# Kernel optimization log

Hardware: AMD Instinct MI355X
Metric: run time of the kernel (lower is better)

The kernel has to match this reference:

```python
import jax, jax.numpy as jnp
import numpy as np

B, C, H, W = 4, 128, 64, 64
HEADS, DH, MEM = 4, 32, 16
HID = HEADS * DH  # 128


def setup_inputs() -> dict:
    key = jax.random.key(0)
    k1, k2, k3, k4, k5 = jax.random.split(key, 5)
    return {
        "x": jax.random.normal(k1, (B, C, H, W), jnp.float32),
        "memory": jax.random.normal(k2, (1, C, 1, MEM), jnp.float32),
        "w_qkv": jax.random.normal(k3, (3 * HID, C), jnp.float32) * 0.05,  # conv1x1, bias=False
        "w_out": jax.random.normal(k4, (C, HID), jnp.float32) * 0.05,      # conv1x1 weight
        "b_out": jax.random.normal(k5, (C,), jnp.float32) * 0.01,          # conv1x1 bias
    }


def reference(x, memory, w_qkv, w_out, b_out):
    b, c, h, w = x.shape
    hw = h * w
    scale = DH ** -0.5

    # flatten spatial, append memory tokens along token axis
    x_flat = x.reshape(b, c, hw)                         # (b, c, hw)
    mem = jnp.broadcast_to(memory[:, :, 0, :], (b, c, MEM))
    x_ext = jnp.concatenate([x_flat, mem], axis=2)       # (b, c, n) n = hw + MEM

    # 1x1 conv QKV projection == channel matmul
    qkv = jnp.einsum('oc,bcn->bon', w_qkv, x_ext)        # (b, 3*HID, n)
    q, k, v = jnp.split(qkv, 3, axis=1)                  # each (b, HID, n)

    def to_heads(t):
        return t.reshape(b, HEADS, DH, -1)               # (b, h, d, n)

    q = to_heads(q) * scale
    k = to_heads(k)
    v = to_heads(v)

    sim = jnp.einsum('bhdi,bhdj->bhij', q, k)            # (b, h, n, n)
    attn = jax.nn.softmax(sim, axis=-1)                  # stable softmax (amax-sub inside)
    out = jnp.einsum('bhij,bhdj->bhid', attn, v)         # (b, h, n, d)

    out = out[:, :, :hw]                                 # drop memory-token queries
    out = out.transpose(0, 1, 3, 2).reshape(b, HID, h, w)  # b (h d) x y

    return jnp.einsum('oc,bchw->bohw', w_out, out) + b_out[None, :, None, None]
```

## Files before the change

### kernel.cpp

```cpp
#include <hip/hip_runtime.h>
#include <hip/hip_bf16.h>

constexpr int NQ   = 4096;
constexpr int NKV  = 4112;
constexpr int NP   = 4160;
constexpr int CDIM = 128;
constexpr int NSL  = 2;
constexpr float QSC = 0.17677669529663687f * 1.4426950408889634f;

typedef __attribute__((ext_vector_type(8)))  short bf16x8;
typedef __attribute__((ext_vector_type(4)))  short bf16x4;
typedef __attribute__((ext_vector_type(4)))  float f32x4;
typedef __attribute__((ext_vector_type(16))) float f32x16;

static __device__ __forceinline__ unsigned short bfbits(float f) {
  __hip_bfloat16 h = __float2bfloat16(f);
  return *reinterpret_cast<unsigned short*>(&h);
}
static __device__ __forceinline__ unsigned pk2(float a, float b) {
  return (unsigned)bfbits(a) | ((unsigned)bfbits(b) << 16);
}

__global__ __launch_bounds__(256) void k1_qkv(
    const float* __restrict__ x, const float* __restrict__ memry,
    const float* __restrict__ wqkv, const float* __restrict__ wout,
    __hip_bfloat16* __restrict__ Qt, __hip_bfloat16* __restrict__ Kt,
    __hip_bfloat16* __restrict__ Vt, __hip_bfloat16* __restrict__ Wb) {
  __shared__ __align__(16) __hip_bfloat16 xt[64][136];
  const int b  = blockIdx.y;
  const int nb = blockIdx.x * 64;
  const int t  = threadIdx.x;
  const int wv = t >> 6, ln = t & 63;

  if (blockIdx.x == 0 && b == 0) {
    for (int i = t; i < CDIM * CDIM; i += 256) Wb[i] = __float2bfloat16(wout[i]);
  }

  {
    const int n = nb + ln;
    #pragma unroll
    for (int i = 0; i < 16; ++i) {
      const int c = wv * 32 + 2 * i;
      float v0 = 0.f, v1 = 0.f;
      if (n < NQ)        { v0 = x[((size_t)b * CDIM + c) * NQ + n];
                           v1 = x[((size_t)b * CDIM + c + 1) * NQ + n]; }
      else if (n < NKV)  { v0 = memry[c * 16 + (n - NQ)];
                           v1 = memry[(c + 1) * 16 + (n - NQ)]; }
      *reinterpret_cast<unsigned*>(&xt[ln][c]) =
          (unsigned)bfbits(v0) | ((unsigned)bfbits(v1) << 16);
    }
  }
  __syncthreads();

  const int li = ln & 15, g = ln >> 4;
  bf16x8 xa[4][4];
  #pragma unroll
  for (int nt = 0; nt < 4; ++nt)
    #pragma unroll
    for (int k = 0; k < 4; ++k)
      xa[nt][k] = *reinterpret_cast<const bf16x8*>(&xt[nt * 16 + li][k * 32 + 8 * g]);

  #pragma unroll
  for (int oi = 0; oi < 6; ++oi) {
    const int ot = wv * 6 + oi;
    bf16x8 wf[4];
    #pragma unroll
    for (int k = 0; k < 4; ++k) {
      const float* wp = &wqkv[(size_t)(ot * 16 + li) * CDIM + k * 32 + 8 * g];
      const float4 f0 = *reinterpret_cast<const float4*>(wp);
      const float4 f1 = *reinterpret_cast<const float4*>(wp + 4);
      bf16x8 wc;
      wc[0] = (short)bfbits(f0.x); wc[1] = (short)bfbits(f0.y);
      wc[2] = (short)bfbits(f0.z); wc[3] = (short)bfbits(f0.w);
      wc[4] = (short)bfbits(f1.x); wc[5] = (short)bfbits(f1.y);
      wc[6] = (short)bfbits(f1.z); wc[7] = (short)bfbits(f1.w);
      wf[k] = wc;
    }
    #pragma unroll
    for (int nt = 0; nt < 4; ++nt) {
      f32x4 a; a[0] = a[1] = a[2] = a[3] = 0.f;
      if (ot < 16) {
        #pragma unroll
        for (int k = 0; k < 4; ++k)
          a = __builtin_amdgcn_mfma_f32_16x16x32_bf16(xa[nt][k], wf[k], a, 0, 0, 0);
        const int o = ot * 16 + li;
        const int h = (o >> 5) & 3, d = o & 31;
        if (ot < 8) {
          #pragma unroll
          for (int r = 0; r < 4; ++r) {
            const int n = nb + nt * 16 + 4 * g + r;
            Qt[((size_t)(b * 4 + h) * NP + n) * 32 + d] = __float2bfloat16(a[r] * QSC);
          }
        } else {
          #pragma unroll
          for (int r = 0; r < 4; ++r) {
            const int n = nb + nt * 16 + 4 * g + r;
            Kt[((size_t)(b * 4 + h) * NP + n) * 32 + d] = __float2bfloat16(a[r]);
          }
        }
      } else {
        #pragma unroll
        for (int k = 0; k < 4; ++k)
          a = __builtin_amdgcn_mfma_f32_16x16x32_bf16(wf[k], xa[nt][k], a, 0, 0, 0);
        #pragma unroll
        for (int r = 0; r < 4; ++r) {
          const int o = ot * 16 + 4 * g + r;
          const int h = (o >> 5) & 3, d = o & 31;
          const int n = nb + nt * 16 + li;
          Vt[((size_t)(b * 4 + h) * 32 + d) * NP + n] = __float2bfloat16(a[r]);
        }
      }
    }
  }
}


#if __has_builtin(__builtin_amdgcn_mfma_f32_32x32x8bf16_1k)
#define HAS_PV8 1
#else
#define HAS_PV8 0
#endif

__global__ __launch_bounds__(256, 4) void k2_attn(
    const __hip_bfloat16* __restrict__ Qt, const __hip_bfloat16* __restrict__ Kt,
    const __hip_bfloat16* __restrict__ Vt, float* __restrict__ Pb,
    float* __restrict__ Lb) {
  __shared__ __align__(16) unsigned char smem[16384];

  const int wg  = blockIdx.x;
  const int xcd = wg & 7;
  const int i   = wg >> 3;
  const int bh  = 2 * xcd + (i & 1);
  const int sl  = (i >> 1) & 1;
  const int wv  = threadIdx.x >> 6, lane = threadIdx.x & 63;
  const int lq  = lane & 31, hi = lane >> 5;
  const int qb  = (i >> 2) * 128 + wv * 32;

  const bf16x8 qf0 = *reinterpret_cast<const bf16x8*>(
      Qt + ((size_t)bh * NP + qb + lq) * 32 + 8 * hi);
  const bf16x8 qf1 = *reinterpret_cast<const bf16x8*>(
      Qt + ((size_t)bh * NP + qb + lq) * 32 + 16 + 8 * hi);

  const int kb0 = sl * 2048;
  const __hip_bfloat16* Ksrc = Kt + ((size_t)bh * NP + kb0 + (wv >> 1) * 32 + lq) * 32
                                  + (wv & 1) * 16 + 8 * hi;
  const __hip_bfloat16* Vsrc = Vt + ((size_t)bh * 32 + lq) * NP + kb0 + wv * 16 + 8 * hi;
  const int dstoff = wv * 1024 + lane * 16;

  f32x16 acc0, acc1, z;
  #pragma unroll
  for (int q = 0; q < 16; ++q) { acc0[q] = 0.f; acc1[q] = 0.f; z[q] = 0.f; }
  float l0 = 0.f, l1 = 0.f, l2 = 0.f, l3 = 0.f;

  bf16x8 kreg = *reinterpret_cast<const bf16x8*>(Ksrc);
  bf16x8 vreg = *reinterpret_cast<const bf16x8*>(Vsrc);
  *reinterpret_cast<bf16x8*>(smem + dstoff)        = kreg;
  *reinterpret_cast<bf16x8*>(smem + 4096 + dstoff) = vreg;
  kreg = *reinterpret_cast<const bf16x8*>(Ksrc + 2048);
  vreg = *reinterpret_cast<const bf16x8*>(Vsrc + 64);

  for (int t = 0; t < 32; ++t) {
    __syncthreads();
    const int p = t & 1;
    if (t < 31) {
      unsigned char* nb = smem + (p ^ 1) * 8192;
      *reinterpret_cast<bf16x8*>(nb + dstoff)        = kreg;
      *reinterpret_cast<bf16x8*>(nb + 4096 + dstoff) = vreg;
      if (t < 30) {
        kreg = *reinterpret_cast<const bf16x8*>(Ksrc + (size_t)(t + 2) * 2048);
        vreg = *reinterpret_cast<const bf16x8*>(Vsrc + (t + 2) * 64);
      }
    }
    const __hip_bfloat16* kbuf = (const __hip_bfloat16*)(smem + p * 8192);
    const __hip_bfloat16* vbuf = (const __hip_bfloat16*)(smem + p * 8192 + 4096);

    #pragma unroll
    for (int st = 0; st < 2; ++st) {
      const bf16x8 kf0 = *reinterpret_cast<const bf16x8*>(kbuf + st * 1024 + lane * 8);
      const bf16x8 kf1 = *reinterpret_cast<const bf16x8*>(kbuf + st * 1024 + 512 + lane * 8);
      f32x16 s = __builtin_amdgcn_mfma_f32_32x32x16_bf16(kf0, qf0, z, 0, 0, 0);
      s = __builtin_amdgcn_mfma_f32_32x32x16_bf16(kf1, qf1, s, 0, 0, 0);
      float p_[16];
      #pragma unroll
      for (int r = 0; r < 16; ++r) p_[r] = __builtin_amdgcn_exp2f(s[r]);
      l0 += (p_[0] + p_[1]) + (p_[2] + p_[3]);
      l1 += (p_[4] + p_[5]) + (p_[6] + p_[7]);
      l2 += (p_[8] + p_[9]) + (p_[10] + p_[11]);
      l3 += (p_[12] + p_[13]) + (p_[14] + p_[15]);
#if HAS_PV8
      union UU { unsigned u[2]; bf16x4 v; };
      UU a0, a1, a2, a3;
      a0.u[0] = pk2(p_[0], p_[1]);   a0.u[1] = pk2(p_[2], p_[3]);
      a1.u[0] = pk2(p_[4], p_[5]);   a1.u[1] = pk2(p_[6], p_[7]);
      a2.u[0] = pk2(p_[8], p_[9]);   a2.u[1] = pk2(p_[10], p_[11]);
      a3.u[0] = pk2(p_[12], p_[13]); a3.u[1] = pk2(p_[14], p_[15]);
      const __hip_bfloat16* vb = vbuf + st * 1024 + lq * 8 + hi * 4;
      const bf16x4 vf0 = *reinterpret_cast<const bf16x4*>(vb);
      const bf16x4 vf1 = *reinterpret_cast<const bf16x4*>(vb + 256);
      const bf16x4 vf2 = *reinterpret_cast<const bf16x4*>(vb + 512);
      const bf16x4 vf3 = *reinterpret_cast<const bf16x4*>(vb + 768);
      acc0 = __builtin_amdgcn_mfma_f32_32x32x8bf16_1k(a0.v, vf0, acc0, 0, 0, 0);
      acc0 = __builtin_amdgcn_mfma_f32_32x32x8bf16_1k(a1.v, vf1, acc0, 0, 0, 0);
      acc1 = __builtin_amdgcn_mfma_f32_32x32x8bf16_1k(a2.v, vf2, acc1, 0, 0, 0);
      acc1 = __builtin_amdgcn_mfma_f32_32x32x8bf16_1k(a3.v, vf3, acc1, 0, 0, 0);
#else
      unsigned a0u0 = pk2(p_[0], p_[1]),   a0u1 = pk2(p_[2], p_[3]);
      unsigned a1u0 = pk2(p_[4], p_[5]),   a1u1 = pk2(p_[6], p_[7]);
      unsigned a2u0 = pk2(p_[8], p_[9]),   a2u1 = pk2(p_[10], p_[11]);
      unsigned a3u0 = pk2(p_[12], p_[13]), a3u1 = pk2(p_[14], p_[15]);
      union U8 { unsigned u[4]; bf16x8 v; };
      const bf16x8 vh0 = *reinterpret_cast<const bf16x8*>(vbuf + (2 * st) * 512 + lane * 8);
      const bf16x8 vh1 = *reinterpret_cast<const bf16x8*>(vbuf + (2 * st + 1) * 512 + lane * 8);
      {
        const unsigned s0 = __shfl_xor(hi ? a0u0 : a1u0, 32, 64);
        const unsigned s1 = __shfl_xor(hi ? a0u1 : a1u1, 32, 64);
        U8 f;
        f.u[0] = hi ? s0 : a0u0; f.u[1] = hi ? s1 : a0u1;
        f.u[2] = hi ? a1u0 : s0; f.u[3] = hi ? a1u1 : s1;
        acc0 = __builtin_amdgcn_mfma_f32_32x32x16_bf16(f.v, vh0, acc0, 0, 0, 0);
      }
      {
        const unsigned s0 = __shfl_xor(hi ? a2u0 : a3u0, 32, 64);
        const unsigned s1 = __shfl_xor(hi ? a2u1 : a3u1, 32, 64);
        U8 f;
        f.u[0] = hi ? s0 : a2u0; f.u[1] = hi ? s1 : a2u1;
        f.u[2] = hi ? a3u0 : s0; f.u[3] = hi ? a3u1 : s1;
        acc1 = __builtin_amdgcn_mfma_f32_32x32x16_bf16(f.v, vh1, acc1, 0, 0, 0);
      }
#endif
    }
  }

  if (sl == NSL - 1) {
    const __hip_bfloat16* Kp   = Kt + (size_t)bh * NP * 32 + (size_t)lq * 32 + 8 * hi;
    const __hip_bfloat16* Vrow = Vt + ((size_t)bh * 32 + lq) * NP;
    const int kb = 4096;
    const bf16x8 kf0 = *reinterpret_cast<const bf16x8*>(Kp + (size_t)kb * 32);
    const bf16x8 kf1 = *reinterpret_cast<const bf16x8*>(Kp + (size_t)kb * 32 + 16);
    f32x16 s = __builtin_amdgcn_mfma_f32_32x32x16_bf16(kf0, qf0, z, 0, 0, 0);
    s = __builtin_amdgcn_mfma_f32_32x32x16_bf16(kf1, qf1, s, 0, 0, 0);
    float p_[8];
    #pragma unroll
    for (int r = 0; r < 8; ++r) p_[r] = __builtin_amdgcn_exp2f(s[r]);
    l0 += (p_[0] + p_[1]) + (p_[2] + p_[3]);
    l1 += (p_[4] + p_[5]) + (p_[6] + p_[7]);
#if HAS_PV8
    union UU { unsigned u[2]; bf16x4 v; };
    UU a0, a1;
    a0.u[0] = pk2(p_[0], p_[1]); a0.u[1] = pk2(p_[2], p_[3]);
    a1.u[0] = pk2(p_[4], p_[5]); a1.u[1] = pk2(p_[6], p_[7]);
    const bf16x4 vf0 = *reinterpret_cast<const bf16x4*>(Vrow + kb + 4 * hi);
    const bf16x4 vf1 = *reinterpret_cast<const bf16x4*>(Vrow + kb + 8 + 4 * hi);
    acc0 = __builtin_amdgcn_mfma_f32_32x32x8bf16_1k(a0.v, vf0, acc0, 0, 0, 0);
    acc0 = __builtin_amdgcn_mfma_f32_32x32x8bf16_1k(a1.v, vf1, acc0, 0, 0, 0);
#else
    unsigned a0u0 = pk2(p_[0], p_[1]), a0u1 = pk2(p_[2], p_[3]);
    unsigned a1u0 = pk2(p_[4], p_[5]), a1u1 = pk2(p_[6], p_[7]);
    union U8 { unsigned u[4]; bf16x8 v; };
    const unsigned s0 = __shfl_xor(hi ? a0u0 : a1u0, 32, 64);
    const unsigned s1 = __shfl_xor(hi ? a0u1 : a1u1, 32, 64);
    U8 f;
    f.u[0] = hi ? s0 : a0u0; f.u[1] = hi ? s1 : a0u1;
    f.u[2] = hi ? a1u0 : s0; f.u[3] = hi ? a1u1 : s1;
    const bf16x8 vf = *reinterpret_cast<const bf16x8*>(Vrow + kb + 8 * hi);
    acc0 = __builtin_amdgcn_mfma_f32_32x32x16_bf16(f.v, vf, acc0, 0, 0, 0);
#endif
  }

  float* Pp = Pb + (((size_t)sl * 16 + bh) * NQ + qb) * 32;
  #pragma unroll
  for (int r = 0; r < 16; ++r) {
    const int q = (r & 3) + 8 * (r >> 2) + 4 * hi;
    Pp[(size_t)q * 32 + lq] = acc0[r] + acc1[r];
  }
  float lsum = (l0 + l1) + (l2 + l3);
  lsum += __shfl_xor(lsum, 32, 64);
  if (hi == 0)
    Lb[((size_t)sl * 16 + bh) * NQ + qb + lq] = lsum;
}

__global__ __launch_bounds__(256) void k2b_combine(
    const float* __restrict__ Pb, const float* __restrict__ Lb,
    __hip_bfloat16* __restrict__ att) {
  const int idx = blockIdx.x * 256 + threadIdx.x;
  const int bh = idx >> 12;
  const int q  = idx & 4095;
  constexpr size_t PS = (size_t)16 * NQ * 32;
  constexpr size_t LS = (size_t)16 * NQ;
  const float* p = Pb + ((size_t)bh * NQ + q) * 32;

  float l = 0.f;
  #pragma unroll
  for (int s = 0; s < NSL; ++s) l += Lb[s * LS + (size_t)bh * NQ + q];
  const float inv = 1.f / l;

  float o[32];
  #pragma unroll
  for (int j = 0; j < 8; ++j) {
    const float4 f = *reinterpret_cast<const float4*>(p + 4 * j);
    o[4*j] = f.x; o[4*j+1] = f.y; o[4*j+2] = f.z; o[4*j+3] = f.w;
  }
  #pragma unroll
  for (int s = 1; s < NSL; ++s)
    #pragma unroll
    for (int j = 0; j < 8; ++j) {
      const float4 f = *reinterpret_cast<const float4*>(p + s * PS + 4 * j);
      o[4*j] += f.x; o[4*j+1] += f.y; o[4*j+2] += f.z; o[4*j+3] += f.w;
    }

  unsigned wb[16];
  #pragma unroll
  for (int j = 0; j < 16; ++j) wb[j] = pk2(o[2*j] * inv, o[2*j+1] * inv);
  __hip_bfloat16* dst = att + ((size_t)bh * NQ + q) * 32;
  *reinterpret_cast<uint4*>(dst)      = make_uint4(wb[0],  wb[1],  wb[2],  wb[3]);
  *reinterpret_cast<uint4*>(dst + 8)  = make_uint4(wb[4],  wb[5],  wb[6],  wb[7]);
  *reinterpret_cast<uint4*>(dst + 16) = make_uint4(wb[8],  wb[9],  wb[10], wb[11]);
  *reinterpret_cast<uint4*>(dst + 24) = make_uint4(wb[12], wb[13], wb[14], wb[15]);
}

__global__ __launch_bounds__(256) void k3_proj(
    const __hip_bfloat16* __restrict__ att, const __hip_bfloat16* __restrict__ Wb,
    const float* __restrict__ bout, float* __restrict__ out) {
  const int b = blockIdx.y, nb = blockIdx.x * 64;
  const int wv = threadIdx.x >> 6, lane = threadIdx.x & 63;
  const int li = lane & 15, g = lane >> 4;

  bf16x8 wf[2][4];
  float bo[2][4];
  #pragma unroll
  for (int tt = 0; tt < 2; ++tt) {
    const int ot = 2 * wv + tt;
    #pragma unroll
    for (int k = 0; k < 4; ++k)
      wf[tt][k] = *reinterpret_cast<const bf16x8*>(
          &Wb[(size_t)(ot * 16 + li) * CDIM + k * 32 + 8 * g]);
    #pragma unroll
    for (int r = 0; r < 4; ++r) bo[tt][r] = bout[ot * 16 + 4 * g + r];
  }
  #pragma unroll
  for (int nt = 0; nt < 4; ++nt) {
    bf16x8 bfr[4];
    #pragma unroll
    for (int k = 0; k < 4; ++k)
      bfr[k] = *reinterpret_cast<const bf16x8*>(
          &att[(((size_t)(b * 4 + k)) * NQ + nb + nt * 16 + li) * 32 + 8 * g]);
    #pragma unroll
    for (int tt = 0; tt < 2; ++tt) {
      f32x4 a; a[0] = a[1] = a[2] = a[3] = 0.f;
      #pragma unroll
      for (int k = 0; k < 4; ++k)
        a = __builtin_amdgcn_mfma_f32_16x16x32_bf16(wf[tt][k], bfr[k], a, 0, 0, 0);
      const int ot = 2 * wv + tt;
      #pragma unroll
      for (int r = 0; r < 4; ++r)
        out[((size_t)b * CDIM + ot * 16 + 4 * g + r) * NQ + nb + nt * 16 + li] =
            a[r] + bo[tt][r];
    }
  }
}

extern "C" void kernel_launch(void* const* d_in, const int* in_sizes, int n_in,
                              void* d_out, int out_size, void* d_ws, size_t ws_size,
                              hipStream_t stream) {
  const float* x    = (const float*)d_in[0];
  const float* memp = (const float*)d_in[1];
  const float* wqkv = (const float*)d_in[2];
  const float* wout = (const float*)d_in[3];
  const float* bout = (const float*)d_in[4];
  float* out = (float*)d_out;

  char* ws = (char*)d_ws;
  const size_t SZ  = (size_t)16 * NP * 32 * 2;
  const size_t PSZ = (size_t)NSL * 16 * NQ * 32 * 4;
  const size_t LSZ = (size_t)NSL * 16 * NQ * 4;
  const size_t ASZ = (size_t)16 * NQ * 32 * 2;
  __hip_bfloat16* Qt  = (__hip_bfloat16*)(ws);
  __hip_bfloat16* Kt  = (__hip_bfloat16*)(ws + SZ);
  __hip_bfloat16* Vt  = (__hip_bfloat16*)(ws + 2 * SZ);
  float*          Pbf = (float*)(ws + 3 * SZ);
  float*          Lbf = (float*)(ws + 3 * SZ + PSZ);
  __hip_bfloat16* att = (__hip_bfloat16*)(ws + 3 * SZ + PSZ + LSZ);
  __hip_bfloat16* Wb  = (__hip_bfloat16*)(ws + 3 * SZ + PSZ + LSZ + ASZ);

  hipLaunchKernelGGL(k1_qkv, dim3(65, 4), dim3(256), 0, stream,
                     x, memp, wqkv, wout, Qt, Kt, Vt, Wb);
  hipLaunchKernelGGL(k2_attn, dim3(1024), dim3(256), 0, stream,
                     Qt, Kt, Vt, Pbf, Lbf);
  hipLaunchKernelGGL(k2b_combine, dim3(256), dim3(256), 0, stream, Pbf, Lbf, att);
  hipLaunchKernelGGL(k3_proj, dim3(64, 4), dim3(256), 0, stream, att, Wb, bout, out);
}
```

Measured before the change: 98.04 us.

## Swizzle attention LDS layout, fuse split-KV combine into projection, widen blocks

The attention kernel now stores K/V tiles in shared memory with an XOR swizzle, plus a half-swap for V rows, to cut LDS bank conflicts on the MFMA operand reads. The separate combine kernel is removed: the output projection now reads the two fp32 partial sums and normaliser arrays directly, merges and normalises them while building its bf16 operands. This saves one launch and the bf16 att round trip. The QKV and projection kernels move to 512-thread blocks with less work per wave. In exchange, the projection kernel reads fp32 partials redundantly across waves, and the swizzle index math adds ALU work.

```diff
diff --git a/kernel.cpp b/kernel.cpp
--- a/kernel.cpp
+++ b/kernel.cpp
@@ -21,7 +21,7 @@
   return (unsigned)bfbits(a) | ((unsigned)bfbits(b) << 16);
 }
 
-__global__ __launch_bounds__(256) void k1_qkv(
+__global__ __launch_bounds__(512) void k1_qkv(
     const float* __restrict__ x, const float* __restrict__ memry,
     const float* __restrict__ wqkv, const float* __restrict__ wout,
     __hip_bfloat16* __restrict__ Qt, __hip_bfloat16* __restrict__ Kt,
@@ -33,14 +33,14 @@
   const int wv = t >> 6, ln = t & 63;
 
   if (blockIdx.x == 0 && b == 0) {
-    for (int i = t; i < CDIM * CDIM; i += 256) Wb[i] = __float2bfloat16(wout[i]);
+    for (int i = t; i < CDIM * CDIM; i += 512) Wb[i] = __float2bfloat16(wout[i]);
   }
 
   {
     const int n = nb + ln;
     #pragma unroll
-    for (int i = 0; i < 16; ++i) {
-      const int c = wv * 32 + 2 * i;
+    for (int i = 0; i < 8; ++i) {
+      const int c = wv * 16 + 2 * i;
       float v0 = 0.f, v1 = 0.f;
       if (n < NQ)        { v0 = x[((size_t)b * CDIM + c) * NQ + n];
                            v1 = x[((size_t)b * CDIM + c + 1) * NQ + n]; }
@@ -61,8 +61,8 @@
       xa[nt][k] = *reinterpret_cast<const bf16x8*>(&xt[nt * 16 + li][k * 32 + 8 * g]);
 
   #pragma unroll
-  for (int oi = 0; oi < 6; ++oi) {
-    const int ot = wv * 6 + oi;
+  for (int oi = 0; oi < 3; ++oi) {
+    const int ot = wv * 3 + oi;
     bf16x8 wf[4];
     #pragma unroll
     for (int k = 0; k < 4; ++k) {
@@ -145,7 +145,19 @@
   const __hip_bfloat16* Ksrc = Kt + ((size_t)bh * NP + kb0 + (wv >> 1) * 32 + lq) * 32
                                   + (wv & 1) * 16 + 8 * hi;
   const __hip_bfloat16* Vsrc = Vt + ((size_t)bh * 32 + lq) * NP + kb0 + wv * 16 + 8 * hi;
-  const int dstoff = wv * 1024 + lane * 16;
+
+  const int rowb  = (lane >> 3) & 7;
+  const int wswz  = (wv * 1024 + lane * 16) ^ (rowb << 4);
+  const bool vswap = rowb & 1;
+  const int krb   = lq * 16 + hi * 512;
+  const int krswz = krb ^ (((krb >> 7) & 7) << 4);
+  int voff[4];
+  #pragma unroll
+  for (int j = 0; j < 4; ++j) {
+    const int vb_ = j * 512 + lq * 16 + hi * 8;
+    const int r_  = (vb_ >> 7) & 7;
+    voff[j] = vb_ ^ (r_ << 4) ^ ((r_ & 1) << 3);
+  }
 
   f32x16 acc0, acc1, z;
   #pragma unroll
@@ -154,8 +166,17 @@
 
   bf16x8 kreg = *reinterpret_cast<const bf16x8*>(Ksrc);
   bf16x8 vreg = *reinterpret_cast<const bf16x8*>(Vsrc);
-  *reinterpret_cast<bf16x8*>(smem + dstoff)        = kreg;
-  *reinterpret_cast<bf16x8*>(smem + 4096 + dstoff) = vreg;
+
+#define WRITE_KV(basep)                                                        \
+  {                                                                            \
+    *reinterpret_cast<bf16x8*>((basep) + wswz) = kreg;                         \
+    bf16x8 vv;                                                                 \
+    vv[0] = vreg[4]; vv[1] = vreg[5]; vv[2] = vreg[6]; vv[3] = vreg[7];        \
+    vv[4] = vreg[0]; vv[5] = vreg[1]; vv[6] = vreg[2]; vv[7] = vreg[3];        \
+    *reinterpret_cast<bf16x8*>((basep) + 4096 + wswz) = vswap ? vv : vreg;     \
+  }
+
+  WRITE_KV(smem)
   kreg = *reinterpret_cast<const bf16x8*>(Ksrc + 2048);
   vreg = *reinterpret_cast<const bf16x8*>(Vsrc + 64);
 
@@ -163,21 +184,19 @@
     __syncthreads();
     const int p = t & 1;
     if (t < 31) {
-      unsigned char* nb = smem + (p ^ 1) * 8192;
-      *reinterpret_cast<bf16x8*>(nb + dstoff)        = kreg;
-      *reinterpret_cast<bf16x8*>(nb + 4096 + dstoff) = vreg;
+      unsigned char* nbuf = smem + (p ^ 1) * 8192;
+      WRITE_KV(nbuf)
       if (t < 30) {
         kreg = *reinterpret_cast<const bf16x8*>(Ksrc + (size_t)(t + 2) * 2048);
         vreg = *reinterpret_cast<const bf16x8*>(Vsrc + (t + 2) * 64);
       }
     }
-    const __hip_bfloat16* kbuf = (const __hip_bfloat16*)(smem + p * 8192);
-    const __hip_bfloat16* vbuf = (const __hip_bfloat16*)(smem + p * 8192 + 4096);
+    const unsigned char* bufb = smem + p * 8192;
 
     #pragma unroll
     for (int st = 0; st < 2; ++st) {
-      const bf16x8 kf0 = *reinterpret_cast<const bf16x8*>(kbuf + st * 1024 + lane * 8);
-      const bf16x8 kf1 = *reinterpret_cast<const bf16x8*>(kbuf + st * 1024 + 512 + lane * 8);
+      const bf16x8 kf0 = *reinterpret_cast<const bf16x8*>(bufb + st * 2048 + krswz);
+      const bf16x8 kf1 = *reinterpret_cast<const bf16x8*>(bufb + st * 2048 + 1024 + krswz);
       f32x16 s = __builtin_amdgcn_mfma_f32_32x32x16_bf16(kf0, qf0, z, 0, 0, 0);
       s = __builtin_amdgcn_mfma_f32_32x32x16_bf16(kf1, qf1, s, 0, 0, 0);
       float p_[16];
@@ -194,11 +213,11 @@
       a1.u[0] = pk2(p_[4], p_[5]);   a1.u[1] = pk2(p_[6], p_[7]);
       a2.u[0] = pk2(p_[8], p_[9]);   a2.u[1] = pk2(p_[10], p_[11]);
       a3.u[0] = pk2(p_[12], p_[13]); a3.u[1] = pk2(p_[14], p_[15]);
-      const __hip_bfloat16* vb = vbuf + st * 1024 + lq * 8 + hi * 4;
-      const bf16x4 vf0 = *reinterpret_cast<const bf16x4*>(vb);
-      const bf16x4 vf1 = *reinterpret_cast<const bf16x4*>(vb + 256);
-      const bf16x4 vf2 = *reinterpret_cast<const bf16x4*>(vb + 512);
-      const bf16x4 vf3 = *reinterpret_cast<const bf16x4*>(vb + 768);
+      const unsigned char* vb = bufb + 4096 + st * 2048;
+      const bf16x4 vf0 = *reinterpret_cast<const bf16x4*>(vb + voff[0]);
+      const bf16x4 vf1 = *reinterpret_cast<const bf16x4*>(vb + voff[1]);
+      const bf16x4 vf2 = *reinterpret_cast<const bf16x4*>(vb + voff[2]);
+      const bf16x4 vf3 = *reinterpret_cast<const bf16x4*>(vb + voff[3]);
       acc0 = __builtin_amdgcn_mfma_f32_32x32x8bf16_1k(a0.v, vf0, acc0, 0, 0, 0);
       acc0 = __builtin_amdgcn_mfma_f32_32x32x8bf16_1k(a1.v, vf1, acc0, 0, 0, 0);
       acc1 = __builtin_amdgcn_mfma_f32_32x32x8bf16_1k(a2.v, vf2, acc1, 0, 0, 0);
@@ -209,15 +228,19 @@
       unsigned a2u0 = pk2(p_[8], p_[9]),   a2u1 = pk2(p_[10], p_[11]);
       unsigned a3u0 = pk2(p_[12], p_[13]), a3u1 = pk2(p_[14], p_[15]);
       union U8 { unsigned u[4]; bf16x8 v; };
-      const bf16x8 vh0 = *reinterpret_cast<const bf16x8*>(vbuf + (2 * st) * 512 + lane * 8);
-      const bf16x8 vh1 = *reinterpret_cast<const bf16x8*>(vbuf + (2 * st + 1) * 512 + lane * 8);
+      const unsigned char* vb = bufb + 4096 + st * 2048;
+      union { bf16x4 h[2]; bf16x8 w; } vh0, vh1;
+      vh0.h[0] = *reinterpret_cast<const bf16x4*>(vb + voff[0]);
+      vh0.h[1] = *reinterpret_cast<const bf16x4*>(vb + voff[1]);
+      vh1.h[0] = *reinterpret_cast<const bf16x4*>(vb + voff[2]);
+      vh1.h[1] = *reinterpret_cast<const bf16x4*>(vb + voff[3]);
       {
         const unsigned s0 = __shfl_xor(hi ? a0u0 : a1u0, 32, 64);
         const unsigned s1 = __shfl_xor(hi ? a0u1 : a1u1, 32, 64);
         U8 f;
         f.u[0] = hi ? s0 : a0u0; f.u[1] = hi ? s1 : a0u1;
         f.u[2] = hi ? a1u0 : s0; f.u[3] = hi ? a1u1 : s1;
-        acc0 = __builtin_amdgcn_mfma_f32_32x32x16_bf16(f.v, vh0, acc0, 0, 0, 0);
+        acc0 = __builtin_amdgcn_mfma_f32_32x32x16_bf16(f.v, vh0.w, acc0, 0, 0, 0);
       }
       {
         const unsigned s0 = __shfl_xor(hi ? a2u0 : a3u0, 32, 64);
@@ -225,11 +248,12 @@
         U8 f;
         f.u[0] = hi ? s0 : a2u0; f.u[1] = hi ? s1 : a2u1;
         f.u[2] = hi ? a3u0 : s0; f.u[3] = hi ? a3u1 : s1;
-        acc1 = __builtin_amdgcn_mfma_f32_32x32x16_bf16(f.v, vh1, acc1, 0, 0, 0);
+        acc1 = __builtin_amdgcn_mfma_f32_32x32x16_bf16(f.v, vh1.w, acc1, 0, 0, 0);
       }
 #endif
     }
   }
+#undef WRITE_KV
 
   if (sl == NSL - 1) {
     const __hip_bfloat16* Kp   = Kt + (size_t)bh * NP * 32 + (size_t)lq * 32 + 8 * hi;
@@ -279,83 +303,58 @@
     Lb[((size_t)sl * 16 + bh) * NQ + qb + lq] = lsum;
 }
 
-__global__ __launch_bounds__(256) void k2b_combine(
+__global__ __launch_bounds__(512) void k3_proj(
     const float* __restrict__ Pb, const float* __restrict__ Lb,
-    __hip_bfloat16* __restrict__ att) {
-  const int idx = blockIdx.x * 256 + threadIdx.x;
-  const int bh = idx >> 12;
-  const int q  = idx & 4095;
+    const __hip_bfloat16* __restrict__ Wb, const float* __restrict__ bout,
+    float* __restrict__ out) {
+  const int b = blockIdx.y, nb = blockIdx.x * 64;
+  const int wv = threadIdx.x >> 6;
+  const int lane = threadIdx.x & 63;
+  const int li = lane & 15, g = lane >> 4;
   constexpr size_t PS = (size_t)16 * NQ * 32;
   constexpr size_t LS = (size_t)16 * NQ;
-  const float* p = Pb + ((size_t)bh * NQ + q) * 32;
-
-  float l = 0.f;
-  #pragma unroll
-  for (int s = 0; s < NSL; ++s) l += Lb[s * LS + (size_t)bh * NQ + q];
-  const float inv = 1.f / l;
-
-  float o[32];
-  #pragma unroll
-  for (int j = 0; j < 8; ++j) {
-    const float4 f = *reinterpret_cast<const float4*>(p + 4 * j);
-    o[4*j] = f.x; o[4*j+1] = f.y; o[4*j+2] = f.z; o[4*j+3] = f.w;
-  }
-  #pragma unroll
-  for (int s = 1; s < NSL; ++s)
-    #pragma unroll
-    for (int j = 0; j < 8; ++j) {
-      const float4 f = *reinterpret_cast<const float4*>(p + s * PS + 4 * j);
-      o[4*j] += f.x; o[4*j+1] += f.y; o[4*j+2] += f.z; o[4*j+3] += f.w;
-    }
-
-  unsigned wb[16];
-  #pragma unroll
-  for (int j = 0; j < 16; ++j) wb[j] = pk2(o[2*j] * inv, o[2*j+1] * inv);
-  __hip_bfloat16* dst = att + ((size_t)bh * NQ + q) * 32;
-  *reinterpret_cast<uint4*>(dst)      = make_uint4(wb[0],  wb[1],  wb[2],  wb[3]);
-  *reinterpret_cast<uint4*>(dst + 8)  = make_uint4(wb[4],  wb[5],  wb[6],  wb[7]);
-  *reinterpret_cast<uint4*>(dst + 16) = make_uint4(wb[8],  wb[9],  wb[10], wb[11]);
-  *reinterpret_cast<uint4*>(dst + 24) = make_uint4(wb[12], wb[13], wb[14], wb[15]);
-}
-
-__global__ __launch_bounds__(256) void k3_proj(
-    const __hip_bfloat16* __restrict__ att, const __hip_bfloat16* __restrict__ Wb,
-    const float* __restrict__ bout, float* __restrict__ out) {
-  const int b = blockIdx.y, nb = blockIdx.x * 64;
-  const int wv = threadIdx.x >> 6, lane = threadIdx.x & 63;
-  const int li = lane & 15, g = lane >> 4;
-
-  bf16x8 wf[2][4];
-  float bo[2][4];
-  #pragma unroll
-  for (int tt = 0; tt < 2; ++tt) {
-    const int ot = 2 * wv + tt;
+
+  bf16x8 wf[4];
+  float bo[4];
+  #pragma unroll
+  for (int k = 0; k < 4; ++k)
+    wf[k] = *reinterpret_cast<const bf16x8*>(
+        &Wb[(size_t)(wv * 16 + li) * CDIM + k * 32 + 8 * g]);
+  #pragma unroll
+  for (int r = 0; r < 4; ++r) bo[r] = bout[wv * 16 + 4 * g + r];
+
+  #pragma unroll
+  for (int nt = 0; nt < 4; ++nt) {
+    const int q = nb + nt * 16 + li;
+    bf16x8 bfr[4];
+    #pragma unroll
+    for (int k = 0; k < 4; ++k) {
+      const size_t qi = (size_t)(b * 4 + k) * NQ + q;
+      const float inv = 1.f / (Lb[qi] + Lb[LS + qi]);
+      const float* pp = Pb + qi * 32 + 8 * g;
+      const float4 a0 = *reinterpret_cast<const float4*>(pp);
+      const float4 a1 = *reinterpret_cast<const float4*>(pp + 4);
+      const float4 c0 = *reinterpret_cast<const float4*>(pp + PS);
+      const float4 c1 = *reinterpret_cast<const float4*>(pp + PS + 4);
+      bf16x8 fr;
+      fr[0] = (short)bfbits((a0.x + c0.x) * inv);
+      fr[1] = (short)bfbits((a0.y + c0.y) * inv);
+      fr[2] = (short)bfbits((a0.z + c0.z) * inv);
+      fr[3] = (short)bfbits((a0.w + c0.w) * inv);
+      fr[4] = (short)bfbits((a1.x + c1.x) * inv);
+      fr[5] = (short)bfbits((a1.y + c1.y) * inv);
+      fr[6] = (short)bfbits((a1.z + c1.z) * inv);
+      fr[7] = (short)bfbits((a1.w + c1.w) * inv);
+      bfr[k] = fr;
+    }
+    f32x4 a; a[0] = a[1] = a[2] = a[3] = 0.f;
     #pragma unroll
     for (int k = 0; k < 4; ++k)
-      wf[tt][k] = *reinterpret_cast<const bf16x8*>(
-          &Wb[(size_t)(ot * 16 + li) * CDIM + k * 32 + 8 * g]);
-    #pragma unroll
-    for (int r = 0; r < 4; ++r) bo[tt][r] = bout[ot * 16 + 4 * g + r];
-  }
-  #pragma unroll
-  for (int nt = 0; nt < 4; ++nt) {
-    bf16x8 bfr[4];
-    #pragma unroll
-    for (int k = 0; k < 4; ++k)
-      bfr[k] = *reinterpret_cast<const bf16x8*>(
-          &att[(((size_t)(b * 4 + k)) * NQ + nb + nt * 16 + li) * 32 + 8 * g]);
-    #pragma unroll
-    for (int tt = 0; tt < 2; ++tt) {
-      f32x4 a; a[0] = a[1] = a[2] = a[3] = 0.f;
-      #pragma unroll
-      for (int k = 0; k < 4; ++k)
-        a = __builtin_amdgcn_mfma_f32_16x16x32_bf16(wf[tt][k], bfr[k], a, 0, 0, 0);
-      const int ot = 2 * wv + tt;
-      #pragma unroll
-      for (int r = 0; r < 4; ++r)
-        out[((size_t)b * CDIM + ot * 16 + 4 * g + r) * NQ + nb + nt * 16 + li] =
-            a[r] + bo[tt][r];
-    }
+      a = __builtin_amdgcn_mfma_f32_16x16x32_bf16(wf[k], bfr[k], a, 0, 0, 0);
+    #pragma unroll
+    for (int r = 0; r < 4; ++r)
+      out[((size_t)b * CDIM + wv * 16 + 4 * g + r) * NQ + nb + nt * 16 + li] =
+          a[r] + bo[r];
   }
 }
 
@@ -373,19 +372,17 @@
   const size_t SZ  = (size_t)16 * NP * 32 * 2;
   const size_t PSZ = (size_t)NSL * 16 * NQ * 32 * 4;
   const size_t LSZ = (size_t)NSL * 16 * NQ * 4;
-  const size_t ASZ = (size_t)16 * NQ * 32 * 2;
   __hip_bfloat16* Qt  = (__hip_bfloat16*)(ws);
   __hip_bfloat16* Kt  = (__hip_bfloat16*)(ws + SZ);
   __hip_bfloat16* Vt  = (__hip_bfloat16*)(ws + 2 * SZ);
   float*          Pbf = (float*)(ws + 3 * SZ);
   float*          Lbf = (float*)(ws + 3 * SZ + PSZ);
-  __hip_bfloat16* att = (__hip_bfloat16*)(ws + 3 * SZ + PSZ + LSZ);
-  __hip_bfloat16* Wb  = (__hip_bfloat16*)(ws + 3 * SZ + PSZ + LSZ + ASZ);
-
-  hipLaunchKernelGGL(k1_qkv, dim3(65, 4), dim3(256), 0, stream,
+  __hip_bfloat16* Wb  = (__hip_bfloat16*)(ws + 3 * SZ + PSZ + LSZ);
+
+  hipLaunchKernelGGL(k1_qkv, dim3(65, 4), dim3(512), 0, stream,
                      x, memp, wqkv, wout, Qt, Kt, Vt, Wb);
   hipLaunchKernelGGL(k2_attn, dim3(1024), dim3(256), 0, stream,
                      Qt, Kt, Vt, Pbf, Lbf);
-  hipLaunchKernelGGL(k2b_combine, dim3(256), dim3(256), 0, stream, Pbf, Lbf, att);
-  hipLaunchKernelGGL(k3_proj, dim3(64, 4), dim3(256), 0, stream, att, Wb, bout, out);
-}
+  hipLaunchKernelGGL(k3_proj, dim3(64, 4), dim3(512), 0, stream,
+                     Pbf, Lbf, Wb, bout, out);
+}
```

New measurement: 99.72 us. Within noise of the previous version (+1.7%).
